# Performance work log

Hardware: AMD Instinct MI355X
Metric: run time of the kernel (lower is better)

The kernel has to match this reference:

```python
import jax, jax.numpy as jnp
import numpy as np

K = 3  # kernel_size=(3,3), flat all-ones structuring element


def _erode(x):
    # flat erosion = sliding-window min, SAME padding with +inf (geodesic)
    return jax.lax.reduce_window(x, float('inf'), jax.lax.min,
                                 (1, 1, K, K), (1, 1, 1, 1), 'SAME')


def _dilate(x):
    # flat dilation = sliding-window max, SAME padding with -inf
    return jax.lax.reduce_window(x, -float('inf'), jax.lax.max,
                                 (1, 1, K, K), (1, 1, 1, 1), 'SAME')


def setup_inputs() -> dict:
    key = jax.random.key(0)
    x = jax.random.uniform(key, (16, 3, 1024, 1024), dtype=jnp.float32)
    return {"x": x}


def reference(x) -> jnp.ndarray:
    # morphological opening: dilation(erosion(x)) with flat 3x3 SE,
    # applied per-channel (kernel repeated over channels in the original)
    return _dilate(_erode(x))
```

## Files before the change

### kernel.cpp

```cpp
#include <hip/hip_runtime.h>


#define W 1024
#define H 1024
#define ROWS 16
#define NT 256

typedef float nvec4 __attribute__((ext_vector_type(4)));

struct Row { float4 m; float l0, l1, r0, r1; };

__global__ __launch_bounds__(NT)
void open3x3_v4(const float* __restrict__ in, float* __restrict__ out) {
    const int t  = threadIdx.x;
    const int c0 = 4 * t;
    const int y0 = blockIdx.x * ROWS;
    const size_t imgoff = (size_t)blockIdx.y * (size_t)(W * H);
    const float* img  = in  + imgoff;
    float*       outp = out + imgoff;

    const float PINF = __builtin_inff();
    const float NINF = -__builtin_inff();
    const bool has_l = (c0 > 0);
    const bool has_r = (c0 + 4 < W);
    const int  cl    = has_l ? c0 - 2 : 0;
    const int  cr    = has_r ? c0 + 4 : W - 4;

    auto load_row = [&](int r) -> Row {
        Row R;
        if (r >= 0 && r < H) {
            const float* p = img + r * W;
            R.m = *(const float4*)(p + c0);
            float2 L  = *(const float2*)(p + cl);
            float2 Rr = *(const float2*)(p + cr);
            R.l0 = has_l ? L.x  : PINF;
            R.l1 = has_l ? L.y  : PINF;
            R.r0 = has_r ? Rr.x : PINF;
            R.r1 = has_r ? Rr.y : PINF;
        } else {
            R.m = make_float4(PINF, PINF, PINF, PINF);
            R.l0 = R.l1 = R.r0 = R.r1 = PINF;
        }
        return R;
    };

    auto hmin6 = [&](const Row& R, float hm[6]) {
        const float x0 = R.l0, x1 = R.l1;
        const float x2 = R.m.x, x3 = R.m.y, x4 = R.m.z, x5 = R.m.w;
        const float x6 = R.r0, x7 = R.r1;
        hm[0] = fminf(fminf(x0, x1), x2);
        hm[1] = fminf(fminf(x1, x2), x3);
        hm[2] = fminf(fminf(x2, x3), x4);
        hm[3] = fminf(fminf(x3, x4), x5);
        hm[4] = fminf(fminf(x4, x5), x6);
        hm[5] = fminf(fminf(x5, x6), x7);
    };

    auto erow = [&](int r, const float a[6], const float b[6], const float c[6], float e[6]) {
        if (r >= 0 && r < H) {
            #pragma unroll
            for (int i = 0; i < 6; i++) e[i] = fminf(fminf(a[i], b[i]), c[i]);
            if (!has_l) e[0] = NINF;
            if (!has_r) e[5] = NINF;
        } else {
            #pragma unroll
            for (int i = 0; i < 6; i++) e[i] = NINF;
        }
    };

    auto hmax4 = [&](const float e[6], float hx[4]) {
        #pragma unroll
        for (int i = 0; i < 4; i++) hx[i] = fmaxf(fmaxf(e[i], e[i + 1]), e[i + 2]);
    };

    Row r0 = load_row(y0 - 2);
    Row r1 = load_row(y0 - 1);
    Row r2 = load_row(y0);
    Row r3 = load_row(y0 + 1);
    Row buf[3];
    buf[0] = load_row(y0 + 2);
    buf[1] = load_row(y0 + 3);
    buf[2] = load_row(y0 + 4);

    float hmA[6], hmB[6], hmC[6], hmD[6];
    hmin6(r0, hmA); hmin6(r1, hmB); hmin6(r2, hmC); hmin6(r3, hmD);
    float e[6], hx0[4], hx1[4], hx2[4];
    erow(y0 - 1, hmA, hmB, hmC, e); hmax4(e, hx0);
    erow(y0,     hmB, hmC, hmD, e); hmax4(e, hx1);
    float hmP[6], hmQ[6], hmR[6];
    #pragma unroll
    for (int i = 0; i < 6; i++) { hmP[i] = hmC[i]; hmQ[i] = hmD[i]; }

    #pragma unroll
    for (int k = 0; k < ROWS; k++) {
        const int y = y0 + k;
        Row cur = buf[k % 3];
        if (k < ROWS - 3) buf[k % 3] = load_row(y + 5);

        hmin6(cur, hmR);
        erow(y + 1, hmP, hmQ, hmR, e);
        hmax4(e, hx2);

        nvec4 o;
        o.x = fmaxf(fmaxf(hx0[0], hx1[0]), hx2[0]);
        o.y = fmaxf(fmaxf(hx0[1], hx1[1]), hx2[1]);
        o.z = fmaxf(fmaxf(hx0[2], hx1[2]), hx2[2]);
        o.w = fmaxf(fmaxf(hx0[3], hx1[3]), hx2[3]);
        __builtin_nontemporal_store(o, (nvec4*)(outp + (size_t)y * W + c0));

        #pragma unroll
        for (int i = 0; i < 4; i++) { hx0[i] = hx1[i]; hx1[i] = hx2[i]; }
        #pragma unroll
        for (int i = 0; i < 6; i++) { hmP[i] = hmQ[i]; hmQ[i] = hmR[i]; }
    }
}

extern "C" void kernel_launch(void* const* d_in, const int* in_sizes, int n_in,
                              void* d_out, int out_size, void* d_ws, size_t ws_size,
                              hipStream_t stream) {
    const float* x = (const float*)d_in[0];
    float* out = (float*)d_out;
    dim3 grid(H / ROWS, 48);
    dim3 block(NT);
    open3x3_v4<<<grid, block, 0, stream>>>(x, out);
}
```

Measured before the change: 348.0 us.

## Stage rows into an LDS ring via async global_load_lds and remap tiles

Replaces per-thread register loads, which also fetched overlapping left and right halo pairs from global memory, with asynchronous global-to-LDS row loads into an 8-slot shared ring. Neighbours are then read from LDS, and manual vmcnt waits plus barriers pipeline row prefetch against compute. Tile indices are also permuted so consecutive blocks are spread across the image. This is meant to cut redundant global halo traffic and keep more loads in flight, at the cost of per-row block barriers and LDS usage that may lower occupancy.

```diff
diff --git a/kernel.cpp b/kernel.cpp
--- a/kernel.cpp
+++ b/kernel.cpp
@@ -4,17 +4,27 @@
 #define W 1024
 #define H 1024
 #define ROWS 16
+#define NTILE (H / ROWS)
 #define NT 256
+#define RING 8
 
-typedef float nvec4 __attribute__((ext_vector_type(4)));
+typedef float f4 __attribute__((ext_vector_type(4)));
+typedef float f2 __attribute__((ext_vector_type(2)));
 
-struct Row { float4 m; float l0, l1, r0, r1; };
+#define WAITV(N) do { asm volatile("s_waitcnt vmcnt(" #N ")" ::: "memory"); \
+                      __builtin_amdgcn_sched_barrier(0); } while (0)
+#define BAR()    do { __builtin_amdgcn_s_barrier(); \
+                      __builtin_amdgcn_sched_barrier(0); } while (0)
 
 __global__ __launch_bounds__(NT)
-void open3x3_v4(const float* __restrict__ in, float* __restrict__ out) {
+void open3x3_v9(const float* __restrict__ in, float* __restrict__ out) {
+    __shared__ float smem[RING][W];
+
     const int t  = threadIdx.x;
     const int c0 = 4 * t;
-    const int y0 = blockIdx.x * ROWS;
+    const int bx = blockIdx.x;
+    const int tile = (bx & 7) * (NTILE / 8) + (bx >> 3);
+    const int y0 = tile * ROWS;
     const size_t imgoff = (size_t)blockIdx.y * (size_t)(W * H);
     const float* img  = in  + imgoff;
     float*       outp = out + imgoff;
@@ -23,49 +33,44 @@
     const float NINF = -__builtin_inff();
     const bool has_l = (c0 > 0);
     const bool has_r = (c0 + 4 < W);
-    const int  cl    = has_l ? c0 - 2 : 0;
-    const int  cr    = has_r ? c0 + 4 : W - 4;
 
-    auto load_row = [&](int r) -> Row {
-        Row R;
-        if (r >= 0 && r < H) {
-            const float* p = img + r * W;
-            R.m = *(const float4*)(p + c0);
-            float2 L  = *(const float2*)(p + cl);
-            float2 Rr = *(const float2*)(p + cr);
-            R.l0 = has_l ? L.x  : PINF;
-            R.l1 = has_l ? L.y  : PINF;
-            R.r0 = has_r ? Rr.x : PINF;
-            R.r1 = has_r ? Rr.y : PINF;
-        } else {
-            R.m = make_float4(PINF, PINF, PINF, PINF);
-            R.l0 = R.l1 = R.r0 = R.r1 = PINF;
-        }
-        return R;
+    const int q = t >> 6;
+
+    auto stage = [&](int r, int slot) {
+        int rc = r < 0 ? 0 : (r > H - 1 ? H - 1 : r);
+        const float* gp = img + (size_t)rc * W + c0;
+        float* lp = &smem[slot][q * 256];
+        __builtin_amdgcn_global_load_lds(gp, lp, 16, 0, 0);
     };
 
-    auto hmin6 = [&](const Row& R, float hm[6]) {
-        const float x0 = R.l0, x1 = R.l1;
-        const float x2 = R.m.x, x3 = R.m.y, x4 = R.m.z, x5 = R.m.w;
-        const float x6 = R.r0, x7 = R.r1;
-        hm[0] = fminf(fminf(x0, x1), x2);
-        hm[1] = fminf(fminf(x1, x2), x3);
-        hm[2] = fminf(fminf(x2, x3), x4);
-        hm[3] = fminf(fminf(x3, x4), x5);
-        hm[4] = fminf(fminf(x4, x5), x6);
-        hm[5] = fminf(fminf(x5, x6), x7);
+    auto hminLDS = [&](int r, int slot, float hm[6]) {
+        const float* rowp = &smem[slot][0];
+        const bool rok = (r >= 0) && (r <= H - 1);
+        f4 m  = *(const f4*)(rowp + c0);
+        f2 L  = *(const f2*)(rowp + (has_l ? c0 - 2 : 0));
+        f2 Rr = *(const f2*)(rowp + (has_r ? c0 + 4 : W - 2));
+        const float x0 = has_l ? L.x : PINF;
+        const float x1 = has_l ? L.y : PINF;
+        const float x2 = m.x, x3 = m.y, x4 = m.z, x5 = m.w;
+        const float x6 = has_r ? Rr.x : PINF;
+        const float x7 = has_r ? Rr.y : PINF;
+        hm[0] = rok ? fminf(fminf(x0, x1), x2) : PINF;
+        hm[1] = rok ? fminf(fminf(x1, x2), x3) : PINF;
+        hm[2] = rok ? fminf(fminf(x2, x3), x4) : PINF;
+        hm[3] = rok ? fminf(fminf(x3, x4), x5) : PINF;
+        hm[4] = rok ? fminf(fminf(x4, x5), x6) : PINF;
+        hm[5] = rok ? fminf(fminf(x5, x6), x7) : PINF;
     };
 
     auto erow = [&](int r, const float a[6], const float b[6], const float c[6], float e[6]) {
-        if (r >= 0 && r < H) {
-            #pragma unroll
-            for (int i = 0; i < 6; i++) e[i] = fminf(fminf(a[i], b[i]), c[i]);
-            if (!has_l) e[0] = NINF;
-            if (!has_r) e[5] = NINF;
-        } else {
-            #pragma unroll
-            for (int i = 0; i < 6; i++) e[i] = NINF;
+        const bool eok = (r >= 0) && (r <= H - 1);
+        #pragma unroll
+        for (int i = 0; i < 6; i++) {
+            float v = fminf(fminf(a[i], b[i]), c[i]);
+            e[i] = eok ? v : NINF;
         }
+        if (!has_l) e[0] = NINF;
+        if (!has_r) e[5] = NINF;
     };
 
     auto hmax4 = [&](const float e[6], float hx[4]) {
@@ -73,17 +78,16 @@
         for (int i = 0; i < 4; i++) hx[i] = fmaxf(fmaxf(e[i], e[i + 1]), e[i + 2]);
     };
 
-    Row r0 = load_row(y0 - 2);
-    Row r1 = load_row(y0 - 1);
-    Row r2 = load_row(y0);
-    Row r3 = load_row(y0 + 1);
-    Row buf[3];
-    buf[0] = load_row(y0 + 2);
-    buf[1] = load_row(y0 + 3);
-    buf[2] = load_row(y0 + 4);
+    stage(y0 - 2, 6); stage(y0 - 1, 7);
+    stage(y0 + 0, 0); stage(y0 + 1, 1);
+    stage(y0 + 2, 2); stage(y0 + 3, 3);
+    stage(y0 + 4, 4); stage(y0 + 5, 5);
+    WAITV(4);
+    BAR();
 
     float hmA[6], hmB[6], hmC[6], hmD[6];
-    hmin6(r0, hmA); hmin6(r1, hmB); hmin6(r2, hmC); hmin6(r3, hmD);
+    hminLDS(y0 - 2, 6, hmA); hminLDS(y0 - 1, 7, hmB);
+    hminLDS(y0,     0, hmC); hminLDS(y0 + 1, 1, hmD);
     float e[6], hx0[4], hx1[4], hx2[4];
     erow(y0 - 1, hmA, hmB, hmC, e); hmax4(e, hx0);
     erow(y0,     hmB, hmC, hmD, e); hmax4(e, hx1);
@@ -94,19 +98,27 @@
     #pragma unroll
     for (int k = 0; k < ROWS; k++) {
         const int y = y0 + k;
-        Row cur = buf[k % 3];
-        if (k < ROWS - 3) buf[k % 3] = load_row(y + 5);
+        int rn = y + 6;
+        if (rn > y0 + ROWS + 1) rn = y0 + ROWS + 1;
+        stage(rn, (k + 6) & 7);
 
-        hmin6(cur, hmR);
+        if (k == 0)      WAITV(4);
+        else if (k == 1) WAITV(5);
+        else if (k == 2) WAITV(6);
+        else if (k == 3) WAITV(7);
+        else             WAITV(8);
+        BAR();
+
+        hminLDS(y + 2, (k + 2) & 7, hmR);
         erow(y + 1, hmP, hmQ, hmR, e);
         hmax4(e, hx2);
 
-        nvec4 o;
+        f4 o;
         o.x = fmaxf(fmaxf(hx0[0], hx1[0]), hx2[0]);
         o.y = fmaxf(fmaxf(hx0[1], hx1[1]), hx2[1]);
         o.z = fmaxf(fmaxf(hx0[2], hx1[2]), hx2[2]);
         o.w = fmaxf(fmaxf(hx0[3], hx1[3]), hx2[3]);
-        __builtin_nontemporal_store(o, (nvec4*)(outp + (size_t)y * W + c0));
+        __builtin_nontemporal_store(o, (f4*)(outp + (size_t)y * W + c0));
 
         #pragma unroll
         for (int i = 0; i < 4; i++) { hx0[i] = hx1[i]; hx1[i] = hx2[i]; }
@@ -120,7 +132,7 @@
                               hipStream_t stream) {
     const float* x = (const float*)d_in[0];
     float* out = (float*)d_out;
-    dim3 grid(H / ROWS, 48);
+    dim3 grid(NTILE, 48);
     dim3 block(NT);
-    open3x3_v4<<<grid, block, 0, stream>>>(x, out);
+    open3x3_v9<<<grid, block, 0, stream>>>(x, out);
 }
```

Result: faster. 338.0 us (-2.9%).
